# Performance work log

Measured on AMD Instinct MI355X. Metric: run time of the kernel, lower is better.

The kernel has to match this reference:

```python
import jax, jax.numpy as jnp
import numpy as np

B, S, E, H = 4, 2048, 1024, 16
Dh = E // H
EPS = 1e-5


def setup_inputs() -> dict:
    key = jax.random.key(0)
    ks = jax.random.split(key, 16)
    w = lambda k, shp: jax.random.normal(k, shp, dtype=jnp.float32) * 0.02
    return {
        "x": jax.random.normal(ks[0], (B, S, E), dtype=jnp.float32),
        "Wq": w(ks[1], (E, E)), "bq": jnp.zeros((E,), jnp.float32),
        "Wk": w(ks[2], (E, E)), "bk": jnp.zeros((E,), jnp.float32),
        "Wv": w(ks[3], (E, E)), "bv": jnp.zeros((E,), jnp.float32),
        "Wo": w(ks[4], (E, E)), "bo": jnp.zeros((E,), jnp.float32),
        "an1_a": jnp.ones((1, S, 1), jnp.float32),
        "an1_b": jnp.zeros((1, S, 1), jnp.float32),
        "W1": w(ks[5], (2 * E, E)), "b1": jnp.zeros((2 * E,), jnp.float32),
        "W2": w(ks[6], (E, 2 * E)), "b2": jnp.zeros((E,), jnp.float32),
        "an2_a": jnp.ones((1, S, 1), jnp.float32),
        "an2_b": jnp.zeros((1, S, 1), jnp.float32),
    }


def adaptive_norm(x, a, b):
    # AdaptiveNorm((1, N_s, 1)): normalize over embedding dim, per-position affine.
    mu = jnp.mean(x, axis=-1, keepdims=True)
    var = jnp.mean(jnp.square(x - mu), axis=-1, keepdims=True)
    return a * (x - mu) * jax.lax.rsqrt(var + EPS) + b


def reference(x, Wq, bq, Wk, bk, Wv, bv, Wo, bo, an1_a, an1_b, W1, b1, W2, b2, an2_a, an2_b):
    scale = 1.0 / np.sqrt(E / H)
    # QKV projections -> (B, S, H, Dh)
    q = (x @ Wq.T + bq).reshape(B, S, H, Dh)
    k = (x @ Wk.T + bk).reshape(B, S, H, Dh)
    v = (x @ Wv.T + bv).reshape(B, S, H, Dh)
    # scaled dot-product attention (materializes B,H,S,S like the original)
    scores = jnp.einsum("bshd,bthd->bhst", q, k) * scale
    probs = jax.nn.softmax(scores, axis=-1)
    attn = jnp.einsum("bhst,bthd->bshd", probs, v).reshape(B, S, E)
    attn = attn @ Wo.T + bo
    # residual + adaptive norm (dropout is identity in eval mode)
    h = adaptive_norm(attn + x, an1_a, an1_b)
    ff = jax.nn.relu(h @ W1.T + b1) @ W2.T + b2
    out = adaptive_norm(ff + h, an2_a, an2_b)
    return out
```

## Files before the change

kernel.cpp:

```cpp
#include <hip/hip_runtime.h>


typedef __attribute__((ext_vector_type(8))) short s16x8;
typedef __attribute__((ext_vector_type(4))) short s16x4;
typedef __attribute__((ext_vector_type(4))) unsigned short u16x4;
typedef __attribute__((ext_vector_type(4))) float f32x4;

__device__ __forceinline__ float bf2f(unsigned short u) {
  unsigned int v = ((unsigned int)u) << 16;
  return __builtin_bit_cast(float, v);
}
__device__ __forceinline__ unsigned short f2bf(float f) {
  unsigned int u = __builtin_bit_cast(unsigned int, f);
  u += 0x7fffu + ((u >> 16) & 1u);
  return (unsigned short)(u >> 16);
}
__device__ __forceinline__ unsigned int pkbf_trunc(float f0, float f1) {
  return __builtin_amdgcn_perm(__builtin_bit_cast(unsigned int, f1),
                               __builtin_bit_cast(unsigned int, f0), 0x07060302u);
}
__device__ __forceinline__ f32x4 mfma16(s16x8 a, s16x8 b, f32x4 c) {
  return __builtin_amdgcn_mfma_f32_16x16x32_bf16(a, b, c, 0, 0, 0);
}
__device__ __forceinline__ void gl2lds16(const unsigned short* g, unsigned short* l) {
  __builtin_amdgcn_global_load_lds(
      (const __attribute__((address_space(1))) unsigned int*)(g),
      (__attribute__((address_space(3))) unsigned int*)(l), 16, 0, 0);
}

__global__ void detect_dtype(const unsigned int* __restrict__ x, int* __restrict__ flag) {
  const int tid = threadIdx.x;
  int cnt = 0;
  for (int i = tid; i < 2048; i += 256) {
    const unsigned e = (x[i] >> 7) & 0xFF;
    cnt += (e >= 100 && e <= 150) ? 1 : 0;
  }
#pragma unroll
  for (int off = 32; off >= 1; off >>= 1) cnt += __shfl_xor(cnt, off);
  __shared__ int red[4];
  if ((tid & 63) == 0) red[tid >> 6] = cnt;
  __syncthreads();
  if (tid == 0) *flag = ((red[0] + red[1] + red[2] + red[3]) > 1536) ? 1 : 0;
}

struct CvtArgs {
  const void* src[17];
  unsigned short* dst[17];
  int cum4[18];
};

__global__ __launch_bounds__(256) void cvt_all(CvtArgs a, const int* __restrict__ flag, int total4) {
  const int i = blockIdx.x * 256 + threadIdx.x;
  if (i >= total4) return;
  int lo = 0, hi = 17;
  while (hi - lo > 1) {
    const int mid = (lo + hi) >> 1;
    if (i >= a.cum4[mid]) lo = mid; else hi = mid;
  }
  const int off4 = i - a.cum4[lo];
  if (*flag) {
    const u16x4* s = (const u16x4*)a.src[lo];
    *(u16x4*)&a.dst[lo][off4 * 4] = s[off4];
  } else {
    const float4* s = (const float4*)a.src[lo];
    const float4 v = s[off4];
    u16x4 o;
    o[0] = f2bf(v.x); o[1] = f2bf(v.y); o[2] = f2bf(v.z); o[3] = f2bf(v.w);
    *(u16x4*)&a.dst[lo][off4 * 4] = o;
  }
}

#define QOFF 8388608L
#define SCALE2 0.18033688011f

template <int EPI>
__global__ __launch_bounds__(512, 1) void gemm2(
    const unsigned short* __restrict__ A, const unsigned short* __restrict__ W,
    const unsigned short* __restrict__ bias, const unsigned short* __restrict__ resid,
    unsigned short* __restrict__ out, int M, int N, int K) {
  extern __shared__ unsigned short sh[];

  const int tid = threadIdx.x;
  const int lane = tid & 63;
  const int wave = tid >> 6;
  const int qd = lane >> 4;
  const int c = lane & 15;
  const int wr = (wave >> 2) * 128;
  const int wc = (wave & 3) * 64;

  const int nx = gridDim.x, ny = gridDim.y;
  const int nwg = nx * ny;
  int lin = blockIdx.y * nx + blockIdx.x;
  lin = (lin & 7) * (nwg >> 3) + (lin >> 3);
  const int by = lin % ny;
  const int bx = lin / ny;
  const long m0 = (long)by * 256;
  const long n0 = (long)bx * 256;

  const int srow = tid >> 3;
  const int scc = ((tid & 7) ^ (srow & 7)) * 8;
  const unsigned short* Asrc = A + (m0 + srow) * (long)K + scc;
  const unsigned short* Wsrc = W + (n0 + srow) * (long)K + scc;
  const int lofs = tid * 8;

  f32x4 acc[8][4] = {};

  const int NT = K >> 6;

  auto stageA = [&](int tt, int q) {
    gl2lds16(Asrc + (long)q * 64 * K + (long)tt * 64,
             sh + (tt & 1) * 32768 + q * 4096 + lofs);
  };
  auto stageB = [&](int tt, int q) {
    gl2lds16(Wsrc + (long)q * 64 * K + (long)tt * 64,
             sh + (tt & 1) * 32768 + 16384 + q * 4096 + lofs);
  };

  stageB(0, 0); stageB(0, 1); stageB(0, 2); stageB(0, 3);
  stageA(0, 0); stageA(0, 2); stageA(0, 1); stageA(0, 3);

  for (int t = 0; t < NT; ++t) {
    const unsigned short* Ab = sh + (t & 1) * 32768;
    const unsigned short* Bb = Ab + 16384;
    const bool dost = (t + 1 < NT);

#pragma unroll
    for (int ph = 0; ph < 4; ++ph) {
      const int qm = ph >> 1, qn = ph & 1;
      if (ph == 0)
        asm volatile("s_waitcnt vmcnt(2)\n\ts_barrier" ::: "memory");
      else if (ph == 2) {
        if (dost) asm volatile("s_waitcnt vmcnt(6)\n\ts_barrier" ::: "memory");
        else      asm volatile("s_waitcnt vmcnt(0)\n\ts_barrier" ::: "memory");
      } else
        asm volatile("s_barrier" ::: "memory");

      s16x8 af[4][2], bfr[2][2];
#pragma unroll
      for (int ks = 0; ks < 2; ++ks) {
#pragma unroll
        for (int mt = 0; mt < 4; ++mt)
          af[mt][ks] = *(const s16x8*)&Ab[(wr + qm * 64 + mt * 16 + c) * 64 +
                                          (((ks * 4 + qd) ^ (c & 7)) * 8)];
#pragma unroll
        for (int nt = 0; nt < 2; ++nt)
          bfr[nt][ks] = *(const s16x8*)&Bb[(wc + qn * 32 + nt * 16 + c) * 64 +
                                           (((ks * 4 + qd) ^ (c & 7)) * 8)];
      }

      if (dost) {
        if (ph == 0) { stageB(t + 1, 0); stageB(t + 1, 1); stageB(t + 1, 2); stageB(t + 1, 3); }
        else if (ph == 1) { stageA(t + 1, 0); stageA(t + 1, 2); }
        else if (ph == 2) { stageA(t + 1, 1); stageA(t + 1, 3); }
      }

      __builtin_amdgcn_s_setprio(1);
#pragma unroll
      for (int mt = 0; mt < 4; ++mt)
#pragma unroll
        for (int nt = 0; nt < 2; ++nt)
#pragma unroll
          for (int ks = 0; ks < 2; ++ks)
            acc[qm * 4 + mt][qn * 2 + nt] =
                mfma16(af[mt][ks], bfr[nt][ks], acc[qm * 4 + mt][qn * 2 + nt]);
      __builtin_amdgcn_s_setprio(0);
    }
  }

#pragma unroll
  for (int nt = 0; nt < 4; ++nt) {
    const int gn = (int)n0 + wc + nt * 16 + c;
    const float bv = bf2f(bias[gn]);
#pragma unroll
    for (int mt = 0; mt < 8; ++mt) {
      const long gmb = m0 + wr + mt * 16 + qd * 4;
      if constexpr (EPI == 2) {
#pragma unroll
        for (int r = 0; r < 4; ++r) {
          const long gm = gmb + r;
          const float v = acc[mt][nt][r] + bv + bf2f(resid[gm * N + gn]);
          out[gm * N + gn] = f2bf(v);
        }
      } else if constexpr (EPI == 3) {
#pragma unroll
        for (int r = 0; r < 4; ++r) {
          const long gm = gmb + r;
          float v = acc[mt][nt][r] + bv;
          v = fmaxf(v, 0.0f);
          out[gm * N + gn] = f2bf(v);
        }
      } else {
        const int seg = gn >> 10;
        const int nn = gn & 1023;
        if (seg == 0) {
#pragma unroll
          for (int r = 0; r < 4; ++r)
            out[(gmb + r) * 1024 + nn] = f2bf((acc[mt][nt][r] + bv) * SCALE2);
        } else if (seg == 1) {
#pragma unroll
          for (int r = 0; r < 4; ++r)
            (out + QOFF)[(gmb + r) * 1024 + nn] = f2bf(acc[mt][nt][r] + bv);
        } else {
          const int h = nn >> 6, d = nn & 63;
          const long b = gmb >> 11;
          const int s = (int)(gmb & 2047);
          s16x4 pv;
#pragma unroll
          for (int r = 0; r < 4; ++r) pv[r] = (short)f2bf(acc[mt][nt][r] + bv);
          *(s16x4*)&(out + 2 * QOFF)[((b * 16 + h) * 64L + d) * 2048 + s] = pv;
        }
      }
    }
  }
}

#define ATT_S 2048

__global__ __launch_bounds__(256)
__attribute__((amdgpu_waves_per_eu(2, 2))) void attn_fwd(
    const unsigned short* __restrict__ Q, const unsigned short* __restrict__ K,
    const unsigned short* __restrict__ VT, unsigned short* __restrict__ O) {
  __shared__ unsigned short SH[24576];
  unsigned short* Kb0 = SH;
  unsigned short* Kb1 = SH + 4096;
  unsigned short* Vb0 = SH + 8192;
  unsigned short* Vb1 = SH + 12288;
  unsigned short* Pl  = SH + 16384;

  const int bh = blockIdx.y;
  const int q0 = blockIdx.x * 256;
  const long b = bh >> 4;
  const int h = bh & 15;
  const unsigned short* Qg = Q + (b * 2048) * 1024 + h * 64;
  const unsigned short* Kg = K + (b * 2048) * 1024 + h * 64;
  const unsigned short* Vg = VT + (long)bh * 64 * 2048;

  const int tid = threadIdx.x;
  const int wave = tid >> 6, lane = tid & 63;
  const int qd = lane >> 4, c = lane & 15;
  const int mb = wave * 32;

  const int srow = tid >> 3;
  const int sccs = ((tid & 7) ^ (srow & 7)) * 8;

  s16x8 qf[2][2][2];
#pragma unroll
  for (int h2 = 0; h2 < 2; ++h2)
#pragma unroll
    for (int mt = 0; mt < 2; ++mt)
#pragma unroll
      for (int ks = 0; ks < 2; ++ks)
        qf[h2][mt][ks] = *(const s16x8*)&Qg[(long)(q0 + h2 * 128 + mb + mt * 16 + c) * 1024 +
                                            ks * 32 + qd * 8];

  s16x8 ones;
#pragma unroll
  for (int i = 0; i < 8; ++i) ones[i] = (short)0x3F80;

  f32x4 oacc[2][4][2] = {};
  f32x4 lacc[2][2] = {};

  gl2lds16(Kg + (long)srow * 1024 + sccs, &Kb0[tid * 8]);
  gl2lds16(Kg + (long)(srow + 32) * 1024 + sccs, &Kb0[(256 + tid) * 8]);
  gl2lds16(Vg + (long)srow * 2048 + sccs, &Vb0[tid * 8]);
  gl2lds16(Vg + (long)(srow + 32) * 2048 + sccs, &Vb0[(256 + tid) * 8]);

  for (int it = 0; it < 32; ++it) {
    const int p = it & 1;
    unsigned short* Kc = p ? Kb1 : Kb0;
    unsigned short* Vc = p ? Vb1 : Vb0;
    unsigned short* Kn = p ? Kb0 : Kb1;
    unsigned short* Vn = p ? Vb0 : Vb1;
    const int kvn = (it < 31) ? (it + 1) * 64 : 31 * 64;
    gl2lds16(Kg + (long)(kvn + srow) * 1024 + sccs, &Kn[tid * 8]);
    gl2lds16(Kg + (long)(kvn + srow + 32) * 1024 + sccs, &Kn[(256 + tid) * 8]);
    gl2lds16(Vg + (long)srow * 2048 + kvn + sccs, &Vn[tid * 8]);
    gl2lds16(Vg + (long)(srow + 32) * 2048 + kvn + sccs, &Vn[(256 + tid) * 8]);

    asm volatile("s_waitcnt vmcnt(4)\n\ts_barrier" ::: "memory");

#pragma unroll
    for (int h2 = 0; h2 < 2; ++h2) {
      f32x4 sacc[4][2] = {};
#pragma unroll
      for (int ks = 0; ks < 2; ++ks) {
        const int ch = ((ks * 4 + qd) ^ (c & 7)) * 8;
        s16x8 kf[4];
#pragma unroll
        for (int tt = 0; tt < 4; ++tt)
          kf[tt] = *(const s16x8*)&Kc[(tt * 16 + c) * 64 + ch];
#pragma unroll
        for (int mt = 0; mt < 2; ++mt)
#pragma unroll
          for (int tt = 0; tt < 4; ++tt)
            sacc[tt][mt] = mfma16(kf[tt], qf[h2][mt][ks], sacc[tt][mt]);
      }

#pragma unroll
      for (int mt = 0; mt < 2; ++mt) {
        const int ml = mb + mt * 16 + c;
#pragma unroll
        for (int tt = 0; tt < 4; ++tt) {
          unsigned int pk[2];
          pk[0] = pkbf_trunc(__builtin_amdgcn_exp2f(sacc[tt][mt][0]),
                             __builtin_amdgcn_exp2f(sacc[tt][mt][1]));
          pk[1] = pkbf_trunc(__builtin_amdgcn_exp2f(sacc[tt][mt][2]),
                             __builtin_amdgcn_exp2f(sacc[tt][mt][3]));
          const int chw = ((tt * 2 + (qd >> 1)) ^ (ml & 7)) * 8 + (qd & 1) * 4;
          *(uint2*)&Pl[ml * 64 + chw] = *(uint2*)pk;
        }
      }
      asm volatile("s_waitcnt lgkmcnt(0)" ::: "memory");

#pragma unroll
      for (int ks = 0; ks < 2; ++ks) {
        const int vch = ((ks * 4 + qd) ^ (c & 7)) * 8;
        s16x8 vf[4], pf[2];
#pragma unroll
        for (int dt = 0; dt < 4; ++dt)
          vf[dt] = *(const s16x8*)&Vc[(dt * 16 + c) * 64 + vch];
#pragma unroll
        for (int mt = 0; mt < 2; ++mt) {
          const int pr = mb + mt * 16 + c;
          pf[mt] = *(const s16x8*)&Pl[pr * 64 + (((ks * 4 + qd) ^ (pr & 7)) * 8)];
        }
#pragma unroll
        for (int mt = 0; mt < 2; ++mt) {
#pragma unroll
          for (int dt = 0; dt < 4; ++dt)
            oacc[h2][dt][mt] = mfma16(vf[dt], pf[mt], oacc[h2][dt][mt]);
          lacc[h2][mt] = mfma16(ones, pf[mt], lacc[h2][mt]);
        }
      }
    }

    asm volatile("s_barrier" ::: "memory");
  }

#pragma unroll
  for (int h2 = 0; h2 < 2; ++h2)
#pragma unroll
    for (int mt = 0; mt < 2; ++mt) {
      const float inv = 1.0f / lacc[h2][mt][0];
      const int s = q0 + h2 * 128 + mb + mt * 16 + c;
      const long ob = (b * (long)ATT_S + s) * 1024L + h * 64;
#pragma unroll
      for (int dt = 0; dt < 4; ++dt) {
        s16x4 ov;
#pragma unroll
        for (int r = 0; r < 4; ++r) ov[r] = (short)f2bf(oacc[h2][dt][mt][r] * inv);
        *(s16x4*)&O[ob + dt * 16 + qd * 4] = ov;
      }
    }
}

template <bool FINAL>
__global__ __launch_bounds__(256) void norm_affine(
    const unsigned short* __restrict__ X, const unsigned short* __restrict__ av,
    const unsigned short* __restrict__ bv, void* __restrict__ outv,
    const int* __restrict__ flag) {
  const int row = blockIdx.x;
  const int s = row & 2047;
  const unsigned short* xr = X + (long)row * 1024;
  const int tid = threadIdx.x;
  const u16x4 u = *(const u16x4*)&xr[tid * 4];
  float v[4];
  float s1 = 0.f, s2 = 0.f;
#pragma unroll
  for (int i = 0; i < 4; ++i) {
    v[i] = bf2f(u[i]);
    s1 += v[i];
    s2 += v[i] * v[i];
  }
#pragma unroll
  for (int off = 32; off >= 1; off >>= 1) {
    s1 += __shfl_xor(s1, off);
    s2 += __shfl_xor(s2, off);
  }
  __shared__ float red[8];
  const int wave = tid >> 6, lane = tid & 63;
  if (lane == 0) {
    red[wave * 2] = s1;
    red[wave * 2 + 1] = s2;
  }
  __syncthreads();
  s1 = red[0] + red[2] + red[4] + red[6];
  s2 = red[1] + red[3] + red[5] + red[7];
  const float mean = s1 * (1.0f / 1024.0f);
  const float var = fmaxf(s2 * (1.0f / 1024.0f) - mean * mean, 0.0f);
  const float rstd = rsqrtf(var + 1e-5f);
  const float aa = bf2f(av[s]), bb = bf2f(bv[s]);
  float o[4];
#pragma unroll
  for (int i = 0; i < 4; ++i) o[i] = aa * (v[i] - mean) * rstd + bb;
  bool as_bf16 = true;
  if constexpr (FINAL) as_bf16 = (*flag != 0);
  if (as_bf16) {
    u16x4 ob;
#pragma unroll
    for (int i = 0; i < 4; ++i) ob[i] = f2bf(o[i]);
    *(u16x4*)&((unsigned short*)outv)[(long)row * 1024 + tid * 4] = ob;
  } else {
    float4 of = {o[0], o[1], o[2], o[3]};
    *(float4*)&((float*)outv)[(long)row * 1024 + tid * 4] = of;
  }
}

extern "C" void kernel_launch(void* const* d_in, const int* in_sizes, int n_in,
                              void* d_out, int out_size, void* d_ws, size_t ws_size,
                              hipStream_t stream) {
  char* ws = (char*)d_ws;
  const size_t SZ = 8192ull * 1024 * 2;
  const size_t WSZ = 1024ull * 1024 * 2;

  unsigned short* xb   = (unsigned short*)(ws);
  unsigned short* qb   = (unsigned short*)(ws + SZ);
  unsigned short* kb   = (unsigned short*)(ws + 2 * SZ);
  unsigned short* vtb  = (unsigned short*)(ws + 3 * SZ);
  unsigned short* attn = (unsigned short*)(ws + 4 * SZ);
  unsigned short* hb   = (unsigned short*)(ws + 5 * SZ);
  unsigned short* r1   = qb;
  unsigned short* ffb  = kb;
  unsigned short* r2   = attn;

  char* wreg = ws + 6 * SZ;
  unsigned short* wqb = (unsigned short*)(wreg);
  unsigned short* w1b = (unsigned short*)(wreg + 4 * WSZ);
  unsigned short* w2b = (unsigned short*)(wreg + 6 * WSZ);
  unsigned short* wob = (unsigned short*)(wreg + 3 * WSZ);
  unsigned short* smal = (unsigned short*)(wreg + 8 * WSZ);
  unsigned short* bqb = smal;
  unsigned short* bkb = smal + 1024;
  unsigned short* bvb = smal + 2048;
  unsigned short* bob = smal + 3072;
  unsigned short* b1b = smal + 4096;
  unsigned short* b2b = smal + 6144;
  unsigned short* a1b = smal + 7168;
  unsigned short* g1b = smal + 9216;
  unsigned short* a2b = smal + 11264;
  unsigned short* g2b = smal + 13312;
  int* flag = (int*)(wreg + 8 * WSZ + 64 * 1024);

  CvtArgs ca;
  unsigned short* wkb = wqb + 1024 * 1024;
  unsigned short* wvb = wqb + 2 * 1024 * 1024;
  unsigned short* dsts[17] = {xb, wqb, bqb, wkb, bkb, wvb, bvb, wob, bob,
                              a1b, g1b, w1b, b1b, w2b, b2b, a2b, g2b};
  ca.cum4[0] = 0;
  for (int i = 0; i < 17; ++i) {
    ca.src[i] = d_in[i];
    ca.dst[i] = dsts[i];
    ca.cum4[i + 1] = ca.cum4[i] + in_sizes[i] / 4;
  }
  const int total4 = ca.cum4[17];

  static bool attr_set = false;
  if (!attr_set) {
    attr_set = true;
    hipFuncSetAttribute(reinterpret_cast<const void*>(gemm2<2>),
                        hipFuncAttributeMaxDynamicSharedMemorySize, 131072);
    hipFuncSetAttribute(reinterpret_cast<const void*>(gemm2<3>),
                        hipFuncAttributeMaxDynamicSharedMemorySize, 131072);
    hipFuncSetAttribute(reinterpret_cast<const void*>(gemm2<4>),
                        hipFuncAttributeMaxDynamicSharedMemorySize, 131072);
  }

  dim3 blk(256);
  dim3 blk512(512);
  const int GLDS = 131072;
  detect_dtype<<<1, blk, 0, stream>>>((const unsigned int*)d_in[0], flag);
  cvt_all<<<(total4 + 255) / 256, blk, 0, stream>>>(ca, flag, total4);

  gemm2<4><<<dim3(12, 32), blk512, GLDS, stream>>>(xb, wqb, bqb, nullptr, qb, 8192, 3072, 1024);
  attn_fwd<<<dim3(8, 64), blk, 0, stream>>>(qb, kb, vtb, attn);
  gemm2<2><<<dim3(4, 32), blk512, GLDS, stream>>>(attn, wob, bob, xb, r1, 8192, 1024, 1024);
  norm_affine<false><<<8192, blk, 0, stream>>>(r1, a1b, g1b, hb, nullptr);
  gemm2<3><<<dim3(8, 32), blk512, GLDS, stream>>>(hb, w1b, b1b, nullptr, ffb, 8192, 2048, 1024);
  gemm2<2><<<dim3(4, 32), blk512, GLDS, stream>>>(ffb, w2b, b2b, hb, r2, 8192, 1024, 2048);
  norm_affine<true><<<8192, blk, 0, stream>>>(r2, a2b, g2b, d_out, flag);
}
```

Measured before the change: 458.9 us.

## Use 128-row tiles with triple buffering for N=1024 GEMMs; restructure K-loop phases

The GEMM kernel is templated on the M tile height. The two N=1024 projection GEMMs (Wo and W2) now use 128-row tiles with a three-stage LDS ring and prefetch two K-steps ahead, which doubles their grid from 128 to 256 workgroups so more of the CUs get work. The 256-row path is reorganised from four quarter-phases into two halves that load B fragments once per K-step and reuse them, with fewer barriers. The trade-off is less reuse per tile for the small-tile path and more LDS per workgroup (144 KB).

```diff
diff --git a/kernel.cpp b/kernel.cpp
--- a/kernel.cpp
+++ b/kernel.cpp
@@ -73,11 +73,13 @@
 #define QOFF 8388608L
 #define SCALE2 0.18033688011f
 
-template <int EPI>
+template <int EPI, int BM>
 __global__ __launch_bounds__(512, 1) void gemm2(
     const unsigned short* __restrict__ A, const unsigned short* __restrict__ W,
     const unsigned short* __restrict__ bias, const unsigned short* __restrict__ resid,
     unsigned short* __restrict__ out, int M, int N, int K) {
+  constexpr int NBUF = (BM == 256) ? 2 : 3;
+  constexpr int BUFE = (BM + 256) * 64;
   extern __shared__ unsigned short sh[];
 
   const int tid = threadIdx.x;
@@ -85,7 +87,7 @@
   const int wave = tid >> 6;
   const int qd = lane >> 4;
   const int c = lane & 15;
-  const int wr = (wave >> 2) * 128;
+  const int wr = (wave >> 2) * (BM / 2);
   const int wc = (wave & 3) * 64;
 
   const int nx = gridDim.x, ny = gridDim.y;
@@ -94,7 +96,7 @@
   lin = (lin & 7) * (nwg >> 3) + (lin >> 3);
   const int by = lin % ny;
   const int bx = lin / ny;
-  const long m0 = (long)by * 256;
+  const long m0 = (long)by * BM;
   const long n0 = (long)bx * 256;
 
   const int srow = tid >> 3;
@@ -103,68 +105,108 @@
   const unsigned short* Wsrc = W + (n0 + srow) * (long)K + scc;
   const int lofs = tid * 8;
 
-  f32x4 acc[8][4] = {};
+  f32x4 acc[BM / 32][4] = {};
 
   const int NT = K >> 6;
 
-  auto stageA = [&](int tt, int q) {
-    gl2lds16(Asrc + (long)q * 64 * K + (long)tt * 64,
-             sh + (tt & 1) * 32768 + q * 4096 + lofs);
+  auto stA = [&](int sel, int tt, int q) {
+    gl2lds16(Asrc + (long)q * 64 * K + (long)tt * 64, sh + sel * BUFE + q * 4096 + lofs);
   };
-  auto stageB = [&](int tt, int q) {
+  auto stB = [&](int sel, int tt, int q) {
     gl2lds16(Wsrc + (long)q * 64 * K + (long)tt * 64,
-             sh + (tt & 1) * 32768 + 16384 + q * 4096 + lofs);
+             sh + sel * BUFE + BM * 64 + q * 4096 + lofs);
   };
 
-  stageB(0, 0); stageB(0, 1); stageB(0, 2); stageB(0, 3);
-  stageA(0, 0); stageA(0, 2); stageA(0, 1); stageA(0, 3);
-
+  if constexpr (BM == 256) {
+    stB(0, 0, 0); stB(0, 0, 1); stB(0, 0, 2); stB(0, 0, 3);
+    stA(0, 0, 0); stA(0, 0, 2); stA(0, 0, 1); stA(0, 0, 3);
+  } else {
+    stB(0, 0, 0); stB(0, 0, 1); stB(0, 0, 2); stB(0, 0, 3); stA(0, 0, 0); stA(0, 0, 1);
+    stB(1, 1, 0); stB(1, 1, 1); stB(1, 1, 2); stB(1, 1, 3); stA(1, 1, 0); stA(1, 1, 1);
+  }
+
+  int cur = 0;
   for (int t = 0; t < NT; ++t) {
-    const unsigned short* Ab = sh + (t & 1) * 32768;
-    const unsigned short* Bb = Ab + 16384;
-    const bool dost = (t + 1 < NT);
-
-#pragma unroll
-    for (int ph = 0; ph < 4; ++ph) {
-      const int qm = ph >> 1, qn = ph & 1;
-      if (ph == 0)
-        asm volatile("s_waitcnt vmcnt(2)\n\ts_barrier" ::: "memory");
-      else if (ph == 2) {
-        if (dost) asm volatile("s_waitcnt vmcnt(6)\n\ts_barrier" ::: "memory");
-        else      asm volatile("s_waitcnt vmcnt(0)\n\ts_barrier" ::: "memory");
-      } else
-        asm volatile("s_barrier" ::: "memory");
-
-      s16x8 af[4][2], bfr[2][2];
-#pragma unroll
-      for (int ks = 0; ks < 2; ++ks) {
-#pragma unroll
-        for (int mt = 0; mt < 4; ++mt)
-          af[mt][ks] = *(const s16x8*)&Ab[(wr + qm * 64 + mt * 16 + c) * 64 +
+    const unsigned short* Ab = sh + cur * BUFE;
+    const unsigned short* Bb = Ab + BM * 64;
+
+    if constexpr (BM == 256) {
+      const bool dost = (t + 1 < NT);
+      const int ns = cur ^ 1;
+      asm volatile("s_waitcnt vmcnt(2)\n\ts_barrier" ::: "memory");
+      s16x8 bfr[4][2], af[4][2];
+#pragma unroll
+      for (int nt = 0; nt < 4; ++nt)
+#pragma unroll
+        for (int ks = 0; ks < 2; ++ks)
+          bfr[nt][ks] = *(const s16x8*)&Bb[(wc + nt * 16 + c) * 64 +
+                                           (((ks * 4 + qd) ^ (c & 7)) * 8)];
+#pragma unroll
+      for (int mt = 0; mt < 4; ++mt)
+#pragma unroll
+        for (int ks = 0; ks < 2; ++ks)
+          af[mt][ks] = *(const s16x8*)&Ab[(wr + mt * 16 + c) * 64 +
                                           (((ks * 4 + qd) ^ (c & 7)) * 8)];
-#pragma unroll
-        for (int nt = 0; nt < 2; ++nt)
-          bfr[nt][ks] = *(const s16x8*)&Bb[(wc + qn * 32 + nt * 16 + c) * 64 +
+      if (dost) { stB(ns, t + 1, 0); stB(ns, t + 1, 1); stB(ns, t + 1, 2); stB(ns, t + 1, 3); }
+      __builtin_amdgcn_s_setprio(1);
+#pragma unroll
+      for (int mt = 0; mt < 4; ++mt)
+#pragma unroll
+        for (int nt = 0; nt < 4; ++nt)
+#pragma unroll
+          for (int ks = 0; ks < 2; ++ks)
+            acc[mt][nt] = mfma16(af[mt][ks], bfr[nt][ks], acc[mt][nt]);
+      __builtin_amdgcn_s_setprio(0);
+      if (dost) asm volatile("s_waitcnt vmcnt(4)\n\ts_barrier" ::: "memory");
+      else      asm volatile("s_waitcnt vmcnt(0)\n\ts_barrier" ::: "memory");
+#pragma unroll
+      for (int mt = 0; mt < 4; ++mt)
+#pragma unroll
+        for (int ks = 0; ks < 2; ++ks)
+          af[mt][ks] = *(const s16x8*)&Ab[(wr + 64 + mt * 16 + c) * 64 +
+                                          (((ks * 4 + qd) ^ (c & 7)) * 8)];
+      if (dost) { stA(ns, t + 1, 0); stA(ns, t + 1, 2); stA(ns, t + 1, 1); stA(ns, t + 1, 3); }
+      __builtin_amdgcn_s_setprio(1);
+#pragma unroll
+      for (int mt = 0; mt < 4; ++mt)
+#pragma unroll
+        for (int nt = 0; nt < 4; ++nt)
+#pragma unroll
+          for (int ks = 0; ks < 2; ++ks)
+            acc[4 + mt][nt] = mfma16(af[mt][ks], bfr[nt][ks], acc[4 + mt][nt]);
+      __builtin_amdgcn_s_setprio(0);
+    } else {
+      if (t + 1 < NT) asm volatile("s_waitcnt vmcnt(6)\n\ts_barrier" ::: "memory");
+      else            asm volatile("s_waitcnt vmcnt(0)\n\ts_barrier" ::: "memory");
+      s16x8 bfr[4][2], af[4][2];
+#pragma unroll
+      for (int nt = 0; nt < 4; ++nt)
+#pragma unroll
+        for (int ks = 0; ks < 2; ++ks)
+          bfr[nt][ks] = *(const s16x8*)&Bb[(wc + nt * 16 + c) * 64 +
                                            (((ks * 4 + qd) ^ (c & 7)) * 8)];
+#pragma unroll
+      for (int mt = 0; mt < 4; ++mt)
+#pragma unroll
+        for (int ks = 0; ks < 2; ++ks)
+          af[mt][ks] = *(const s16x8*)&Ab[(wr + mt * 16 + c) * 64 +
+                                          (((ks * 4 + qd) ^ (c & 7)) * 8)];
+      if (t + 2 < NT) {
+        const int ns = (cur >= 1) ? cur - 1 : 2;
+        stB(ns, t + 2, 0); stB(ns, t + 2, 1); stB(ns, t + 2, 2); stB(ns, t + 2, 3);
+        stA(ns, t + 2, 0); stA(ns, t + 2, 1);
       }
-
-      if (dost) {
-        if (ph == 0) { stageB(t + 1, 0); stageB(t + 1, 1); stageB(t + 1, 2); stageB(t + 1, 3); }
-        else if (ph == 1) { stageA(t + 1, 0); stageA(t + 1, 2); }
-        else if (ph == 2) { stageA(t + 1, 1); stageA(t + 1, 3); }
-      }
-
       __builtin_amdgcn_s_setprio(1);
 #pragma unroll
       for (int mt = 0; mt < 4; ++mt)
 #pragma unroll
-        for (int nt = 0; nt < 2; ++nt)
+        for (int nt = 0; nt < 4; ++nt)
 #pragma unroll
           for (int ks = 0; ks < 2; ++ks)
-            acc[qm * 4 + mt][qn * 2 + nt] =
-                mfma16(af[mt][ks], bfr[nt][ks], acc[qm * 4 + mt][qn * 2 + nt]);
+            acc[mt][nt] = mfma16(af[mt][ks], bfr[nt][ks], acc[mt][nt]);
       __builtin_amdgcn_s_setprio(0);
     }
+    cur = (cur + 1 == NBUF) ? 0 : cur + 1;
   }
 
 #pragma unroll
@@ -172,7 +214,7 @@
     const int gn = (int)n0 + wc + nt * 16 + c;
     const float bv = bf2f(bias[gn]);
 #pragma unroll
-    for (int mt = 0; mt < 8; ++mt) {
+    for (int mt = 0; mt < BM / 32; ++mt) {
       const long gmb = m0 + wr + mt * 16 + qd * 4;
       if constexpr (EPI == 2) {
 #pragma unroll
@@ -457,25 +499,24 @@
   static bool attr_set = false;
   if (!attr_set) {
     attr_set = true;
-    hipFuncSetAttribute(reinterpret_cast<const void*>(gemm2<2>),
+    hipFuncSetAttribute(reinterpret_cast<const void*>(gemm2<4, 256>),
                         hipFuncAttributeMaxDynamicSharedMemorySize, 131072);
-    hipFuncSetAttribute(reinterpret_cast<const void*>(gemm2<3>),
+    hipFuncSetAttribute(reinterpret_cast<const void*>(gemm2<3, 256>),
                         hipFuncAttributeMaxDynamicSharedMemorySize, 131072);
-    hipFuncSetAttribute(reinterpret_cast<const void*>(gemm2<4>),
-                        hipFuncAttributeMaxDynamicSharedMemorySize, 131072);
+    hipFuncSetAttribute(reinterpret_cast<const void*>(gemm2<2, 128>),
+                        hipFuncAttributeMaxDynamicSharedMemorySize, 147456);
   }
 
   dim3 blk(256);
   dim3 blk512(512);
-  const int GLDS = 131072;
   detect_dtype<<<1, blk, 0, stream>>>((const unsigned int*)d_in[0], flag);
   cvt_all<<<(total4 + 255) / 256, blk, 0, stream>>>(ca, flag, total4);
 
-  gemm2<4><<<dim3(12, 32), blk512, GLDS, stream>>>(xb, wqb, bqb, nullptr, qb, 8192, 3072, 1024);
+  gemm2<4, 256><<<dim3(12, 32), blk512, 131072, stream>>>(xb, wqb, bqb, nullptr, qb, 8192, 3072, 1024);
   attn_fwd<<<dim3(8, 64), blk, 0, stream>>>(qb, kb, vtb, attn);
-  gemm2<2><<<dim3(4, 32), blk512, GLDS, stream>>>(attn, wob, bob, xb, r1, 8192, 1024, 1024);
+  gemm2<2, 128><<<dim3(4, 64), blk512, 147456, stream>>>(attn, wob, bob, xb, r1, 8192, 1024, 1024);
   norm_affine<false><<<8192, blk, 0, stream>>>(r1, a1b, g1b, hb, nullptr);
-  gemm2<3><<<dim3(8, 32), blk512, GLDS, stream>>>(hb, w1b, b1b, nullptr, ffb, 8192, 2048, 1024);
-  gemm2<2><<<dim3(4, 32), blk512, GLDS, stream>>>(ffb, w2b, b2b, hb, r2, 8192, 1024, 2048);
+  gemm2<3, 256><<<dim3(8, 32), blk512, 131072, stream>>>(hb, w1b, b1b, nullptr, ffb, 8192, 2048, 1024);
+  gemm2<2, 128><<<dim3(4, 64), blk512, 147456, stream>>>(ffb, w2b, b2b, hb, r2, 8192, 1024, 2048);
   norm_affine<true><<<8192, blk, 0, stream>>>(r2, a2b, g2b, d_out, flag);
 }
```

Measured after the change: 404.4 us. 11.9% less time.
